# Kernel tuning notes

Hardware: AMD Instinct MI355X
Metric: run time of the kernel (lower is better)

Reference implementation:

```python
import jax, jax.numpy as jnp
import numpy as np

N_HEAD = 12

def setup_inputs() -> dict:
    key = jax.random.key(0)
    k1, k2, k3 = jax.random.split(key, 3)
    B, T, C = 2, 4096, 768
    x = jax.random.normal(k1, (B, T, C), dtype=jnp.float32)
    Wqkv = jax.random.normal(k2, (C, 3 * C), dtype=jnp.float32) * (1.0 / np.sqrt(C))
    bqkv = jnp.zeros((3 * C,), dtype=jnp.float32)
    Wout = jax.random.normal(k3, (C, C), dtype=jnp.float32) * (1.0 / np.sqrt(C))
    bout = jnp.zeros((C,), dtype=jnp.float32)
    return {"x": x, "Wqkv": Wqkv, "bqkv": bqkv, "Wout": Wout, "bout": bout}

def reference(x, Wqkv, bqkv, Wout, bout):
    B, T, C = x.shape
    H = N_HEAD
    D = C // H
    qkv = x @ Wqkv + bqkv                       # [B,T,3C]
    qkv = qkv.reshape(B, T, 3, H, D)
    q = qkv[:, :, 0].transpose(0, 2, 1, 3)       # [B,H,T,D]
    k = qkv[:, :, 1].transpose(0, 2, 1, 3)
    v = qkv[:, :, 2].transpose(0, 2, 1, 3)
    att = jnp.einsum('bhqd,bhkd->bhqk', q, k) / jnp.sqrt(jnp.float32(D))
    causal = jnp.tril(jnp.ones((T, T), dtype=bool))
    att = jnp.where(causal[None, None], att, jnp.float32(-jnp.inf))
    att = jax.nn.softmax(att, axis=-1)
    out = jnp.einsum('bhqk,bhkd->bhqd', att, v)  # [B,H,T,D]
    out = out.transpose(0, 2, 1, 3).reshape(B, T, C)
    return out @ Wout + bout
```

## Files before the change

### kernel.cpp

```cpp
#include <hip/hip_runtime.h>
#include <math.h>

#define Bb 2
#define Tt 4096
#define Cc 768
#define Hh 12
#define Dd 64

typedef __attribute__((ext_vector_type(8))) short short8;
typedef __attribute__((ext_vector_type(4))) float f32x4;
typedef __attribute__((ext_vector_type(4))) unsigned short u16x4;

static __device__ __forceinline__ unsigned short f2bf(float f) {
    unsigned u = __float_as_uint(f);
    u += 0x7FFF + ((u >> 16) & 1);
    return (unsigned short)(u >> 16);
}

static __device__ __forceinline__ float ex2(float x) {
    return __builtin_amdgcn_exp2f(x);
}

static __device__ __forceinline__ void gload16(const void* g, void* l) {
    __builtin_amdgcn_global_load_lds(
        (const __attribute__((address_space(1))) unsigned*)g,
        (__attribute__((address_space(3))) unsigned*)l, 16, 0, 0);
}

__global__ __launch_bounds__(256)
void cvt_bf16(const float* __restrict__ in, unsigned short* __restrict__ out, int n8) {
    int i = blockIdx.x * 256 + threadIdx.x;
    if (i >= n8) return;
    float4 a = *(const float4*)(in + (size_t)i * 8);
    float4 b = *(const float4*)(in + (size_t)i * 8 + 4);
    union { short8 v; unsigned short u[8]; } p;
    p.u[0] = f2bf(a.x); p.u[1] = f2bf(a.y); p.u[2] = f2bf(a.z); p.u[3] = f2bf(a.w);
    p.u[4] = f2bf(b.x); p.u[5] = f2bf(b.y); p.u[6] = f2bf(b.z); p.u[7] = f2bf(b.w);
    *(short8*)(out + (size_t)i * 8) = p.v;
}

__global__ __launch_bounds__(256)
void transpose_w(const float* __restrict__ W, unsigned short* __restrict__ Wt,
                 int K, int N) {
    __shared__ __align__(16) unsigned short Tl[64][72];
    int n0 = blockIdx.x * 64, k0 = blockIdx.y * 64;
    int t = threadIdx.x;
    int r = t >> 2, c = (t & 3) * 16;
    const float* wp = W + (size_t)(k0 + r) * N + n0 + c;
    #pragma unroll
    for (int j = 0; j < 16; j += 4) {
        float4 v = *(const float4*)(wp + j);
        Tl[c + j + 0][r] = f2bf(v.x);
        Tl[c + j + 1][r] = f2bf(v.y);
        Tl[c + j + 2][r] = f2bf(v.z);
        Tl[c + j + 3][r] = f2bf(v.w);
    }
    __syncthreads();
    unsigned short* op = Wt + (size_t)(n0 + r) * K + k0 + c;
    *(short8*)op       = *(const short8*)&Tl[r][c];
    *(short8*)(op + 8) = *(const short8*)&Tl[r][c + 8];
}

template<bool BF16OUT>
__global__ __launch_bounds__(256)
void gemm_mfma(const unsigned short* __restrict__ A, const unsigned short* __restrict__ Bt,
               const float* __restrict__ bias, void* __restrict__ Cout,
               int M, int N, int K, int qcols,
               unsigned short* __restrict__ vtb, int voff) {
    union SmemU {
        unsigned short ab[2][128][64];
        unsigned short tv[128][136];
    };
    __shared__ __align__(16) SmemU sh;
    const int tid = threadIdx.x;
    const int wid = tid >> 6, lane = tid & 63;
    const int lr = lane & 15, g = lane >> 4;
    const int wr = wid >> 1, wc = wid & 1;
    const int m0 = blockIdx.y * 128, n0 = blockIdx.x * 128;
    const int srow = lane >> 3;
    const int scol = (lane & 7) * 8;

    f32x4 acc[4][4] = {};

    for (int k0 = 0; k0 < K; k0 += 64) {
        #pragma unroll
        for (int j = 0; j < 4; ++j) {
            int ci = wid * 4 + j;
            int row = ci * 8 + srow;
            gload16(A  + (size_t)(m0 + row) * K + k0 + scol, &sh.ab[0][ci * 8][0]);
            gload16(Bt + (size_t)(n0 + row) * K + k0 + scol, &sh.ab[1][ci * 8][0]);
        }
        __syncthreads();
        #pragma unroll
        for (int ks = 0; ks < 2; ++ks) {
            short8 af[4], bfr[4];
            #pragma unroll
            for (int m = 0; m < 4; ++m)
                af[m] = *(const short8*)&sh.ab[0][wr * 64 + m * 16 + lr][ks * 32 + g * 8];
            #pragma unroll
            for (int n = 0; n < 4; ++n)
                bfr[n] = *(const short8*)&sh.ab[1][wc * 64 + n * 16 + lr][ks * 32 + g * 8];
            #pragma unroll
            for (int m = 0; m < 4; ++m)
                #pragma unroll
                for (int n = 0; n < 4; ++n)
                    acc[m][n] = __builtin_amdgcn_mfma_f32_16x16x32_bf16(
                        af[m], bfr[n], acc[m][n], 0, 0, 0);
        }
        __syncthreads();
    }

    if (vtb != nullptr && n0 >= voff) {
        #pragma unroll
        for (int n = 0; n < 4; ++n) {
            int tcol = wc * 64 + n * 16 + lr;
            float bv = bias[n0 + tcol];
            #pragma unroll
            for (int m = 0; m < 4; ++m) {
                int trow = wr * 64 + m * 16 + g * 4;
                #pragma unroll
                for (int r = 0; r < 4; ++r)
                    sh.tv[tcol][trow + r] = f2bf(acc[m][n][r] + bv);
            }
        }
        __syncthreads();
        const int dlocal = tid >> 1;
        const int th     = (tid & 1) * 64;
        const int colg   = n0 + dlocal;
        const int hd     = (colg - voff) >> 6;
        const int d      = (colg - voff) & 63;
        const int token  = m0 + th;
        const int bq     = token >> 12;
        const int t0     = token & (Tt - 1);
        unsigned short* dst = vtb + ((size_t)(bq * Hh + hd) * Dd + d) * Tt + t0;
        const unsigned short* src = &sh.tv[dlocal][th];
        #pragma unroll
        for (int j = 0; j < 8; ++j)
            *(short8*)(dst + j * 8) = *(const short8*)(src + j * 8);
        return;
    }

    const float qscale = 0.125f * 1.44269504088896340736f;
    #pragma unroll
    for (int n = 0; n < 4; ++n) {
        int coln = n0 + wc * 64 + n * 16 + lr;
        float bv = bias[coln];
        float sc = (coln < qcols) ? qscale : 1.0f;
        #pragma unroll
        for (int m = 0; m < 4; ++m) {
            int rowb = m0 + wr * 64 + m * 16 + g * 4;
            #pragma unroll
            for (int r = 0; r < 4; ++r) {
                float v = (acc[m][n][r] + bv) * sc;
                if (BF16OUT)
                    ((unsigned short*)Cout)[(size_t)(rowb + r) * N + coln] = f2bf(v);
                else
                    ((float*)Cout)[(size_t)(rowb + r) * N + coln] = v;
            }
        }
    }
}

__global__ __launch_bounds__(256)
void attn_mfma(const unsigned short* __restrict__ qkvb,
               const unsigned short* __restrict__ vtb,
               unsigned short* __restrict__ outb) {
    const int nid  = blockIdx.x;
    const int xcd  = nid & 7;
    const int rest = nid >> 3;
    const int P    = rest & 31;
    const int H2   = xcd + 8 * (rest >> 5);
    const int hd   = H2 % Hh;
    const int b    = H2 / Hh;
    const int tid = threadIdx.x;
    const int wid = tid >> 6, lane = tid & 63;
    const int lr = lane & 15, g = lane >> 4;
    const int rm7 = lr & 7;
    const size_t rs = 3 * Cc;

    __shared__ __align__(16) unsigned short Ks[3][64 * 64];
    __shared__ __align__(16) unsigned short Vs[3][64 * 64];

    const unsigned short* qkvbase = qkvb + (size_t)b * Tt * rs;
    const unsigned short* vbase   = vtb + (size_t)((b * Hh + hd) * Dd) * Tt;

    const int srw  = lane >> 3;
    const int row0 = wid * 8 + srw;
    const int slog = (lane & 7) ^ (srw & 7);
    const unsigned short* ksrc0 = qkvbase + (size_t)row0 * rs + Cc + hd * Dd + slog * 8;
    const unsigned short* vsrc0 = vbase + (size_t)row0 * Tt + slog * 8;

    const int ntA = 64 - P;
    const int qA  = (63 - P) * 64 + wid * 16 + lr;
    const int qB  = P * 64 + wid * 16 + lr;

    short8 qfA0, qfA1, qfB0, qfB1;
    {
        const unsigned short* qp = qkvbase + (size_t)qA * rs + hd * Dd;
        qfA0 = *(const short8*)(qp + g * 8);
        qfA1 = *(const short8*)(qp + 32 + g * 8);
        qp = qkvbase + (size_t)qB * rs + hd * Dd;
        qfB0 = *(const short8*)(qp + g * 8);
        qfB1 = *(const short8*)(qp + 32 + g * 8);
    }

    auto stage = [&](int buf, int ts) {
        int t = (ts < ntA) ? ts : ts - ntA;
        gload16(ksrc0 + (size_t)t * 64 * rs,        &Ks[buf][wid * 512]);
        gload16(ksrc0 + (size_t)(t * 64 + 32) * rs, &Ks[buf][2048 + wid * 512]);
        gload16(vsrc0 + t * 64,                     &Vs[buf][wid * 512]);
        gload16(vsrc0 + (size_t)32 * Tt + t * 64,   &Vs[buf][2048 + wid * 512]);
    };

    stage(0, 0);
    stage(1, 1);

    const int laneA = lr + ((g & 1) << 5);
    const int laneB = laneA + 16;
    const int asel  = g >> 1;

    f32x4 o[4];
    #pragma unroll
    for (int dt = 0; dt < 4; ++dt) o[dt] = (f32x4){0.f, 0.f, 0.f, 0.f};
    float lpart = 0.f;
    short8 qf0 = qfA0, qf1 = qfA1;
    int myq = qA;

    auto epilogue = [&]() {
        float l_r = lpart;
        l_r += __shfl_xor(l_r, 16);
        l_r += __shfl_xor(l_r, 32);
        float inv = 1.f / fmaxf(l_r, 1e-37f);
        unsigned short* op = outb + ((size_t)b * Tt + myq) * Cc + hd * Dd + g * 4;
        #pragma unroll
        for (int dt = 0; dt < 4; ++dt) {
            u16x4 w;
            #pragma unroll
            for (int r = 0; r < 4; ++r) w[r] = f2bf(o[dt][r] * inv);
            *(u16x4*)(op + dt * 16) = w;
        }
    };

    #pragma unroll 1
    for (int ts = 0; ts < 65; ++ts) {
        if (ts < 64) asm volatile("s_waitcnt vmcnt(4)" ::: "memory");
        else         asm volatile("s_waitcnt vmcnt(0)" ::: "memory");
        __builtin_amdgcn_s_barrier();
        __builtin_amdgcn_sched_barrier(0);
        if (ts + 2 < 65) stage((ts + 2) % 3, ts + 2);

        const int inA = (ts < ntA) ? 1 : 0;
        const int kbt = inA ? ts : ts - ntA;
        const int nt  = inA ? ntA : (65 - ntA);
        const unsigned short* Kc = &Ks[ts % 3][0];
        const unsigned short* Vc = &Vs[ts % 3][0];

        f32x4 st[4];
        __builtin_amdgcn_s_setprio(1);
        #pragma unroll
        for (int kt = 0; kt < 4; ++kt) {
            int row = kt * 16 + lr;
            int off0 = row * 64 + (g ^ rm7) * 8;
            short8 kf0 = *(const short8*)&Kc[off0];
            short8 kf1 = *(const short8*)&Kc[off0 ^ 32];
            f32x4 a = (f32x4){0.f, 0.f, 0.f, 0.f};
            a = __builtin_amdgcn_mfma_f32_16x16x32_bf16(kf0, qf0, a, 0, 0, 0);
            a = __builtin_amdgcn_mfma_f32_16x16x32_bf16(kf1, qf1, a, 0, 0, 0);
            st[kt] = a;
        }
        __builtin_amdgcn_s_setprio(0);

        if (kbt == nt - 1) {
            #pragma unroll
            for (int kt = 0; kt < 4; ++kt)
                #pragma unroll
                for (int r = 0; r < 4; ++r)
                    if (kbt * 64 + kt * 16 + g * 4 + r > myq) st[kt][r] = -1e30f;
        }

        float psum = 0.f;
        #pragma unroll
        for (int kt = 0; kt < 4; ++kt)
            #pragma unroll
            for (int r = 0; r < 4; ++r) {
                float p = ex2(st[kt][r]);
                st[kt][r] = p;
                psum += p;
            }
        lpart += psum;

        unsigned up[4][2];
        #pragma unroll
        for (int kt = 0; kt < 4; ++kt) {
            asm("v_cvt_pk_bf16_f32 %0, %1, %2"
                : "=v"(up[kt][0]) : "v"(st[kt][0]), "v"(st[kt][1]));
            asm("v_cvt_pk_bf16_f32 %0, %1, %2"
                : "=v"(up[kt][1]) : "v"(st[kt][2]), "v"(st[kt][3]));
        }
        #pragma unroll
        for (int ks = 0; ks < 2; ++ks) {
            unsigned wa0 = __shfl(up[2 * ks][0],     laneA);
            unsigned wb0 = __shfl(up[2 * ks + 1][0], laneA);
            unsigned wa1 = __shfl(up[2 * ks][1],     laneA);
            unsigned wb1 = __shfl(up[2 * ks + 1][1], laneA);
            unsigned wa2 = __shfl(up[2 * ks][0],     laneB);
            unsigned wb2 = __shfl(up[2 * ks + 1][0], laneB);
            unsigned wa3 = __shfl(up[2 * ks][1],     laneB);
            unsigned wb3 = __shfl(up[2 * ks + 1][1], laneB);
            union { unsigned w[4]; short8 v; } pb;
            pb.w[0] = asel ? wb0 : wa0;
            pb.w[1] = asel ? wb1 : wa1;
            pb.w[2] = asel ? wb2 : wa2;
            pb.w[3] = asel ? wb3 : wa3;
            __builtin_amdgcn_s_setprio(1);
            #pragma unroll
            for (int dt = 0; dt < 4; ++dt) {
                int row = dt * 16 + lr;
                int off = row * 64 + (((ks << 2) | g) ^ rm7) * 8;
                short8 vf = *(const short8*)&Vc[off];
                o[dt] = __builtin_amdgcn_mfma_f32_16x16x32_bf16(vf, pb.v, o[dt], 0, 0, 0);
            }
            __builtin_amdgcn_s_setprio(0);
        }

        if (ts == ntA - 1) {
            epilogue();
            #pragma unroll
            for (int dt = 0; dt < 4; ++dt) o[dt] = (f32x4){0.f, 0.f, 0.f, 0.f};
            lpart = 0.f;
            qf0 = qfB0; qf1 = qfB1;
            myq = qB;
        }
    }

    epilogue();
}

extern "C" void kernel_launch(void* const* d_in, const int* in_sizes, int n_in,
                              void* d_out, int out_size, void* d_ws, size_t ws_size,
                              hipStream_t stream) {
    const float* x    = (const float*)d_in[0];
    const float* Wqkv = (const float*)d_in[1];
    const float* bqkv = (const float*)d_in[2];
    const float* Wout = (const float*)d_in[3];
    const float* bout = (const float*)d_in[4];
    float* out = (float*)d_out;

    const int M = Bb * Tt;
    const int N1 = 3 * Cc;

    char* p = (char*)d_ws;
    unsigned short* qkvb  = (unsigned short*)p; p += (size_t)M * N1 * 2;
    unsigned short* xb    = (unsigned short*)p; p += (size_t)M * Cc * 2;
    unsigned short* wqkvt = (unsigned short*)p; p += (size_t)N1 * Cc * 2;
    unsigned short* woutt = (unsigned short*)p; p += (size_t)Cc * Cc * 2;
    unsigned short* vtb   = (unsigned short*)p; p += (size_t)Bb * Hh * Dd * Tt * 2;
    unsigned short* attb  = (unsigned short*)p; p += (size_t)M * Cc * 2;

    cvt_bf16<<<dim3((M * Cc / 8 + 255) / 256), dim3(256), 0, stream>>>(x, xb, M * Cc / 8);
    transpose_w<<<dim3(N1 / 64, Cc / 64), dim3(256), 0, stream>>>(Wqkv, wqkvt, Cc, N1);
    transpose_w<<<dim3(Cc / 64, Cc / 64), dim3(256), 0, stream>>>(Wout, woutt, Cc, Cc);

    gemm_mfma<true><<<dim3(N1 / 128, M / 128), dim3(256), 0, stream>>>(
        xb, wqkvt, bqkv, qkvb, M, N1, Cc, Cc, vtb, 2 * Cc);

    attn_mfma<<<dim3(32 * Hh * Bb), dim3(256), 0, stream>>>(qkvb, vtb, attb);

    gemm_mfma<false><<<dim3(Cc / 128, M / 128), dim3(256), 0, stream>>>(
        attb, woutt, bout, out, M, Cc, Cc, 0, nullptr, 1 << 30);
}
```

Before: 201.3 us.

## Split attention key tile across two wave groups and combine partial outputs in LDS

Doubles the attention block to 512 threads. Each group of four waves handles half of every 64-key tile, and the two groups' partial O and row sums are merged through shared memory at each epilogue. The K/V pipeline moves from a triple-buffered, explicit vmcnt scheme to double buffering with a __syncthreads per tile. The goal is more waves in flight and less serial work per wave, at the price of extra block-wide barriers, a shallower prefetch, and LDS combine traffic.

```diff
diff --git a/kernel.cpp b/kernel.cpp
--- a/kernel.cpp
+++ b/kernel.cpp
@@ -161,7 +161,7 @@
     }
 }
 
-__global__ __launch_bounds__(256)
+__global__ __launch_bounds__(512)
 void attn_mfma(const unsigned short* __restrict__ qkvb,
                const unsigned short* __restrict__ vtb,
                unsigned short* __restrict__ outb) {
@@ -174,25 +174,27 @@
     const int b    = H2 / Hh;
     const int tid = threadIdx.x;
     const int wid = tid >> 6, lane = tid & 63;
+    const int strip = wid & 3, kh = wid >> 2;
     const int lr = lane & 15, g = lane >> 4;
     const int rm7 = lr & 7;
     const size_t rs = 3 * Cc;
 
-    __shared__ __align__(16) unsigned short Ks[3][64 * 64];
-    __shared__ __align__(16) unsigned short Vs[3][64 * 64];
+    __shared__ __align__(16) unsigned short Ks[2][64 * 64];
+    __shared__ __align__(16) unsigned short Vs[2][64 * 64];
+    __shared__ __align__(16) float combO[4][64][16];
+    __shared__ float combL[4][64];
 
     const unsigned short* qkvbase = qkvb + (size_t)b * Tt * rs;
     const unsigned short* vbase   = vtb + (size_t)((b * Hh + hd) * Dd) * Tt;
 
-    const int srw  = lane >> 3;
-    const int row0 = wid * 8 + srw;
-    const int slog = (lane & 7) ^ (srw & 7);
+    const int row0 = tid >> 3;
+    const int slog = (tid & 7) ^ (row0 & 7);
     const unsigned short* ksrc0 = qkvbase + (size_t)row0 * rs + Cc + hd * Dd + slog * 8;
     const unsigned short* vsrc0 = vbase + (size_t)row0 * Tt + slog * 8;
 
     const int ntA = 64 - P;
-    const int qA  = (63 - P) * 64 + wid * 16 + lr;
-    const int qB  = P * 64 + wid * 16 + lr;
+    const int qA  = (63 - P) * 64 + strip * 16 + lr;
+    const int qB  = P * 64 + strip * 16 + lr;
 
     short8 qfA0, qfA1, qfB0, qfB1;
     {
@@ -206,14 +208,13 @@
 
     auto stage = [&](int buf, int ts) {
         int t = (ts < ntA) ? ts : ts - ntA;
-        gload16(ksrc0 + (size_t)t * 64 * rs,        &Ks[buf][wid * 512]);
-        gload16(ksrc0 + (size_t)(t * 64 + 32) * rs, &Ks[buf][2048 + wid * 512]);
-        gload16(vsrc0 + t * 64,                     &Vs[buf][wid * 512]);
-        gload16(vsrc0 + (size_t)32 * Tt + t * 64,   &Vs[buf][2048 + wid * 512]);
+        gload16(ksrc0 + (size_t)t * 64 * rs, &Ks[buf][wid * 512]);
+        gload16(vsrc0 + t * 64,              &Vs[buf][wid * 512]);
     };
 
     stage(0, 0);
-    stage(1, 1);
+    __syncthreads();
+    int cur = 0;
 
     const int laneA = lr + ((g & 1) << 5);
     const int laneB = laneA + 16;
@@ -226,40 +227,47 @@
     short8 qf0 = qfA0, qf1 = qfA1;
     int myq = qA;
 
-    auto epilogue = [&]() {
-        float l_r = lpart;
-        l_r += __shfl_xor(l_r, 16);
-        l_r += __shfl_xor(l_r, 32);
-        float inv = 1.f / fmaxf(l_r, 1e-37f);
-        unsigned short* op = outb + ((size_t)b * Tt + myq) * Cc + hd * Dd + g * 4;
-        #pragma unroll
-        for (int dt = 0; dt < 4; ++dt) {
-            u16x4 w;
-            #pragma unroll
-            for (int r = 0; r < 4; ++r) w[r] = f2bf(o[dt][r] * inv);
-            *(u16x4*)(op + dt * 16) = w;
-        }
+    auto combine_epilogue = [&]() {
+        if (kh) {
+            #pragma unroll
+            for (int dt = 0; dt < 4; ++dt)
+                *(f32x4*)&combO[strip][lane][dt * 4] = o[dt];
+            combL[strip][lane] = lpart;
+        }
+        __syncthreads();
+        if (!kh) {
+            float l_r = lpart + combL[strip][lane];
+            l_r += __shfl_xor(l_r, 16);
+            l_r += __shfl_xor(l_r, 32);
+            float inv = 1.f / fmaxf(l_r, 1e-37f);
+            unsigned short* op = outb + ((size_t)b * Tt + myq) * Cc + hd * Dd + g * 4;
+            #pragma unroll
+            for (int dt = 0; dt < 4; ++dt) {
+                f32x4 t2 = *(const f32x4*)&combO[strip][lane][dt * 4];
+                u16x4 w;
+                #pragma unroll
+                for (int r = 0; r < 4; ++r) w[r] = f2bf((o[dt][r] + t2[r]) * inv);
+                *(u16x4*)(op + dt * 16) = w;
+            }
+        }
+        __syncthreads();
     };
 
     #pragma unroll 1
     for (int ts = 0; ts < 65; ++ts) {
-        if (ts < 64) asm volatile("s_waitcnt vmcnt(4)" ::: "memory");
-        else         asm volatile("s_waitcnt vmcnt(0)" ::: "memory");
-        __builtin_amdgcn_s_barrier();
-        __builtin_amdgcn_sched_barrier(0);
-        if (ts + 2 < 65) stage((ts + 2) % 3, ts + 2);
+        if (ts + 1 < 65) stage(cur ^ 1, ts + 1);
 
         const int inA = (ts < ntA) ? 1 : 0;
         const int kbt = inA ? ts : ts - ntA;
         const int nt  = inA ? ntA : (65 - ntA);
-        const unsigned short* Kc = &Ks[ts % 3][0];
-        const unsigned short* Vc = &Vs[ts % 3][0];
-
-        f32x4 st[4];
+        const unsigned short* Kc = &Ks[cur][0];
+        const unsigned short* Vc = &Vs[cur][0];
+
+        f32x4 st[2];
         __builtin_amdgcn_s_setprio(1);
         #pragma unroll
-        for (int kt = 0; kt < 4; ++kt) {
-            int row = kt * 16 + lr;
+        for (int kt = 0; kt < 2; ++kt) {
+            int row = kh * 32 + kt * 16 + lr;
             int off0 = row * 64 + (g ^ rm7) * 8;
             short8 kf0 = *(const short8*)&Kc[off0];
             short8 kf1 = *(const short8*)&Kc[off0 ^ 32];
@@ -272,15 +280,16 @@
 
         if (kbt == nt - 1) {
             #pragma unroll
-            for (int kt = 0; kt < 4; ++kt)
+            for (int kt = 0; kt < 2; ++kt)
                 #pragma unroll
                 for (int r = 0; r < 4; ++r)
-                    if (kbt * 64 + kt * 16 + g * 4 + r > myq) st[kt][r] = -1e30f;
+                    if (kbt * 64 + kh * 32 + kt * 16 + g * 4 + r > myq)
+                        st[kt][r] = -1e30f;
         }
 
         float psum = 0.f;
         #pragma unroll
-        for (int kt = 0; kt < 4; ++kt)
+        for (int kt = 0; kt < 2; ++kt)
             #pragma unroll
             for (int r = 0; r < 4; ++r) {
                 float p = ex2(st[kt][r]);
@@ -289,24 +298,23 @@
             }
         lpart += psum;
 
-        unsigned up[4][2];
-        #pragma unroll
-        for (int kt = 0; kt < 4; ++kt) {
+        unsigned up[2][2];
+        #pragma unroll
+        for (int kt = 0; kt < 2; ++kt) {
             asm("v_cvt_pk_bf16_f32 %0, %1, %2"
                 : "=v"(up[kt][0]) : "v"(st[kt][0]), "v"(st[kt][1]));
             asm("v_cvt_pk_bf16_f32 %0, %1, %2"
                 : "=v"(up[kt][1]) : "v"(st[kt][2]), "v"(st[kt][3]));
         }
-        #pragma unroll
-        for (int ks = 0; ks < 2; ++ks) {
-            unsigned wa0 = __shfl(up[2 * ks][0],     laneA);
-            unsigned wb0 = __shfl(up[2 * ks + 1][0], laneA);
-            unsigned wa1 = __shfl(up[2 * ks][1],     laneA);
-            unsigned wb1 = __shfl(up[2 * ks + 1][1], laneA);
-            unsigned wa2 = __shfl(up[2 * ks][0],     laneB);
-            unsigned wb2 = __shfl(up[2 * ks + 1][0], laneB);
-            unsigned wa3 = __shfl(up[2 * ks][1],     laneB);
-            unsigned wb3 = __shfl(up[2 * ks + 1][1], laneB);
+        {
+            unsigned wa0 = __shfl(up[0][0], laneA);
+            unsigned wb0 = __shfl(up[1][0], laneA);
+            unsigned wa1 = __shfl(up[0][1], laneA);
+            unsigned wb1 = __shfl(up[1][1], laneA);
+            unsigned wa2 = __shfl(up[0][0], laneB);
+            unsigned wb2 = __shfl(up[1][0], laneB);
+            unsigned wa3 = __shfl(up[0][1], laneB);
+            unsigned wb3 = __shfl(up[1][1], laneB);
             union { unsigned w[4]; short8 v; } pb;
             pb.w[0] = asel ? wb0 : wa0;
             pb.w[1] = asel ? wb1 : wa1;
@@ -316,15 +324,18 @@
             #pragma unroll
             for (int dt = 0; dt < 4; ++dt) {
                 int row = dt * 16 + lr;
-                int off = row * 64 + (((ks << 2) | g) ^ rm7) * 8;
+                int off = row * 64 + (((kh << 2) | g) ^ rm7) * 8;
                 short8 vf = *(const short8*)&Vc[off];
                 o[dt] = __builtin_amdgcn_mfma_f32_16x16x32_bf16(vf, pb.v, o[dt], 0, 0, 0);
             }
             __builtin_amdgcn_s_setprio(0);
         }
 
+        __syncthreads();
+        cur ^= 1;
+
         if (ts == ntA - 1) {
-            epilogue();
+            combine_epilogue();
             #pragma unroll
             for (int dt = 0; dt < 4; ++dt) o[dt] = (f32x4){0.f, 0.f, 0.f, 0.f};
             lpart = 0.f;
@@ -333,7 +344,7 @@
         }
     }
 
-    epilogue();
+    combine_epilogue();
 }
 
 extern "C" void kernel_launch(void* const* d_in, const int* in_sizes, int n_in,
@@ -364,7 +375,7 @@
     gemm_mfma<true><<<dim3(N1 / 128, M / 128), dim3(256), 0, stream>>>(
         xb, wqkvt, bqkv, qkvb, M, N1, Cc, Cc, vtb, 2 * Cc);
 
-    attn_mfma<<<dim3(32 * Hh * Bb), dim3(256), 0, stream>>>(qkvb, vtb, attb);
+    attn_mfma<<<dim3(32 * Hh * Bb), dim3(512), 0, stream>>>(qkvb, vtb, attb);
 
     gemm_mfma<false><<<dim3(Cc / 128, M / 128), dim3(256), 0, stream>>>(
         attb, woutt, bout, out, M, Cc, Cc, 0, nullptr, 1 << 30);
```

After: 194.2 us. 1.04x faster.
